# Performance work log

Measured on AMD Instinct MI355X. Metric: run time of the kernel, lower is better.

The kernel has to match this reference:

```python
import jax, jax.numpy as jnp
import numpy as np

B, K, V, NB = 256, 62, 14522, 28

def setup_inputs() -> dict:
    key = jax.random.key(0)
    ks = jax.random.split(key, 10)
    thetas = jax.random.normal(ks[0], (B, K * 3), dtype=jnp.float32) * 0.2
    bone_lengths_core = jax.random.normal(ks[1], (B, NB), dtype=jnp.float32)
    center_bone_length = jax.random.uniform(ks[2], (B, 1), dtype=jnp.float32) + 0.5
    trans = jax.random.normal(ks[3], (B, 3), dtype=jnp.float32)
    scale = jax.random.uniform(ks[4], (B,), dtype=jnp.float32) + 0.5
    v_template = jax.random.normal(ks[5], (V, 3), dtype=jnp.float32) * 0.05
    t_pose_joints = jax.random.normal(ks[6], (K, 3), dtype=jnp.float32) * 0.1
    weights = jax.nn.softmax(jax.random.normal(ks[7], (V, K), dtype=jnp.float32) * 2.0, axis=1)
    # kinematic tree: parent[i] < i (binary-ish tree), parent[0] unused
    parents = jnp.maximum((jnp.arange(K) - 1) // 2, 0).astype(jnp.int64)
    bone_length_mapper = jax.random.randint(ks[8], (K,), -1, NB).astype(jnp.int64)
    return {"thetas": thetas, "bone_lengths_core": bone_lengths_core,
            "center_bone_length": center_bone_length, "trans": trans, "scale": scale,
            "v_template": v_template, "t_pose_joints": t_pose_joints, "weights": weights,
            "parents": parents, "bone_length_mapper": bone_length_mapper}

def euler2mat(r):
    # r: [N,3] ZYX euler angles -> [N,3,3]
    z, y, x = r[:, 0], r[:, 1], r[:, 2]
    cx, sx = jnp.cos(x), jnp.sin(x)
    cy, sy = jnp.cos(y), jnp.sin(y)
    cz, sz = jnp.cos(z), jnp.sin(z)
    one = jnp.ones_like(x)
    zero = jnp.zeros_like(x)
    Rx = jnp.stack([one, zero, zero, zero, cx, -sx, zero, sx, cx], -1).reshape(-1, 3, 3)
    Ry = jnp.stack([cy, zero, sy, zero, one, zero, -sy, zero, cy], -1).reshape(-1, 3, 3)
    Rz = jnp.stack([cz, -sz, zero, sz, cz, zero, zero, zero, one], -1).reshape(-1, 3, 3)
    return jnp.einsum('nij,njk,nkl->nil', Rz, Ry, Rx)

def _forward(thetas, bone_lengths_core, center_bone_length, trans, scale,
             v_template, t_pose_joints, weights, parents, bone_length_mapper):
    b = thetas.shape[0]
    k = t_pose_joints.shape[0]
    blc = jax.nn.sigmoid(bone_lengths_core / 5.0) * 2.0          # [B,28]
    R = euler2mat(thetas.reshape(-1, 3)).reshape(b, k, 3, 3)      # [B,K,3,3]
    Jt = t_pose_joints                                            # [K,3]
    # per-joint bone-length scale factor [B,K]
    gathered = blc[:, jnp.clip(bone_length_mapper, 0)]            # [B,K]
    factor = jnp.where(bone_length_mapper[None, :] < 0, 1.0, gathered)
    factor = factor.at[:, 1].set(center_bone_length[:, 0])
    factor = factor.at[:, 0].set(1.0)
    # local translations: root uses J0, others scaled offsets to parent
    off = (Jt - Jt[parents])[None] * factor[:, :, None]           # [B,K,3]
    off = off.at[:, 0].set(Jt[0][None])
    # local affines A [B,K,4,4]
    A = jnp.zeros((b, k, 4, 4), dtype=thetas.dtype)
    A = A.at[:, :, :3, :3].set(R)
    A = A.at[:, :, :3, 3].set(off)
    A = A.at[:, :, 3, 3].set(1.0)
    # compose along the kinematic tree
    G0 = jnp.zeros_like(A).at[:, 0].set(A[:, 0])
    def step(G_all, i):
        Gp = jnp.take(G_all, parents[i], axis=1)                  # [B,4,4]
        Gi = Gp @ jnp.take(A, i, axis=1)
        return jax.lax.dynamic_update_index_in_dim(G_all, Gi, i, axis=1), None
    G_all, _ = jax.lax.scan(step, G0, jnp.arange(1, k))
    J_final = G_all[:, :, :3, 3]                                  # [B,K,3]
    # subtract inverse-bind contribution: G' = G - pack(G @ [J;0])
    RJ = jnp.einsum('bkij,kj->bki', G_all[:, :, :3, :3], Jt)
    G = G_all.at[:, :, :3, 3].add(-RJ)
    # LBS skinning: T [B,V,4,4]
    T = jnp.einsum('bkij,vk->bvij', G, weights)
    rest_h = jnp.concatenate([v_template, jnp.ones((v_template.shape[0], 1), v_template.dtype)], axis=1)
    v = jnp.einsum('bvij,vj->bvi', T, rest_h)[:, :, :3]
    V_final = v * scale[:, None, None] + trans[:, None, :]
    J_out = J_final * scale[:, None, None] + trans[:, None, :]
    return V_final, J_out

def reference(thetas, bone_lengths_core, center_bone_length, trans, scale,
              v_template, t_pose_joints, weights, parents, bone_length_mapper):
    return _forward(thetas, bone_lengths_core, center_bone_length, trans, scale,
                    v_template, t_pose_joints, weights, parents, bone_length_mapper)
```

## Files before the change

### kernel.cpp

```cpp
#include <hip/hip_runtime.h>

#define NBATCH 256
#define NJ     62
#define NV     14522
#define NCORE  28
#define KPAD   256
#define NN     768
#define MPAD   14528
#define OUTF   (NV * 3)
#define MT     908
#define NSTRIPE 128

typedef __attribute__((ext_vector_type(8))) short short8v;
typedef __attribute__((ext_vector_type(4))) short short4v;
typedef __attribute__((ext_vector_type(4))) float floatx4;
typedef __attribute__((ext_vector_type(2))) float floatx2;

#define AS1(p) ((const __attribute__((address_space(1))) void*)(p))
#define AS3(p) ((__attribute__((address_space(3))) void*)(p))

#define SCHED0() __builtin_amdgcn_sched_barrier(0)
#define WAITVM(n) do { SCHED0(); asm volatile("s_waitcnt vmcnt(" #n ")" ::: "memory"); SCHED0(); } while (0)

static __device__ inline short f2bf(float x) {
    unsigned u = __float_as_uint(x);
    unsigned r = (u + 0x7fffu + ((u >> 16) & 1u)) >> 16;
    return (short)r;
}

static __device__ inline unsigned swz(unsigned off) {
    return off ^ (((off >> 9) & 7u) << 4);
}

__global__ __launch_bounds__(256) void prep_kernel(
    const float* __restrict__ thetas, const float* __restrict__ blc,
    const float* __restrict__ cbl, const float* __restrict__ trans,
    const float* __restrict__ scale, const float* __restrict__ tpose,
    const int* __restrict__ parents, const int* __restrict__ mapper,
    const float* __restrict__ W, const float* __restrict__ vt,
    short* __restrict__ Bt, short* __restrict__ WH,
    float* __restrict__ Jout)
{
    __shared__ float Asm[4][NJ][12];
    __shared__ float Gsm[4][NJ][12];

    if (blockIdx.x >= 64) {
        const int id = (blockIdx.x - 64) * 256 + threadIdx.x;
        const int v = id >> 5;
        const int c = id & 31;
        const int k = c * 2;
        float w0 = 0.f, w1 = 0.f, hx = 0.f, hy = 0.f, hz = 0.f;
        if (v < NV) {
            hx = vt[v * 3 + 0]; hy = vt[v * 3 + 1]; hz = vt[v * 3 + 2];
            if (k < NJ)     w0 = W[(size_t)v * NJ + k];
            if (k + 1 < NJ) w1 = W[(size_t)v * NJ + k + 1];
        }
        short8v o;
        o[0] = f2bf(w0 * hx); o[1] = f2bf(w0 * hy); o[2] = f2bf(w0 * hz); o[3] = f2bf(w0);
        o[4] = f2bf(w1 * hx); o[5] = f2bf(w1 * hy); o[6] = f2bf(w1 * hz); o[7] = f2bf(w1);
        if (v < MPAD) *(short8v*)&WH[(size_t)v * KPAD + c * 8] = o;
        return;
    }

    const int w = threadIdx.x >> 6;
    const int b = blockIdx.x * 4 + w;
    const int k = threadIdx.x & 63;
    int p = 0;

    if (k < NJ) {
        p = parents[k];
        const float tz = thetas[(b * NJ + k) * 3 + 0];
        const float ty = thetas[(b * NJ + k) * 3 + 1];
        const float tx = thetas[(b * NJ + k) * 3 + 2];
        const float cx = cosf(tx), sx = sinf(tx);
        const float cy = cosf(ty), sy = sinf(ty);
        const float cz = cosf(tz), sz = sinf(tz);
        const float r00 = cz * cy;
        const float r01 = cz * sy * sx - sz * cx;
        const float r02 = sz * sx + cz * sy * cx;
        const float r10 = sz * cy;
        const float r11 = cz * cx + sz * sy * sx;
        const float r12 = sz * sy * cx - cz * sx;
        const float r20 = -sy;
        const float r21 = cy * sx;
        const float r22 = cy * cx;

        float f;
        const int m = mapper[k];
        if (k == 0)        f = 1.0f;
        else if (k == 1)   f = cbl[b];
        else if (m < 0)    f = 1.0f;
        else               f = 2.0f / (1.0f + expf(-blc[b * NCORE + m] * 0.2f));

        float ox, oy, oz;
        if (k == 0) {
            ox = tpose[0]; oy = tpose[1]; oz = tpose[2];
        } else {
            ox = (tpose[k * 3 + 0] - tpose[p * 3 + 0]) * f;
            oy = (tpose[k * 3 + 1] - tpose[p * 3 + 1]) * f;
            oz = (tpose[k * 3 + 2] - tpose[p * 3 + 2]) * f;
        }
        Asm[w][k][0] = r00; Asm[w][k][1] = r01; Asm[w][k][2]  = r02; Asm[w][k][3]  = ox;
        Asm[w][k][4] = r10; Asm[w][k][5] = r11; Asm[w][k][6]  = r12; Asm[w][k][7]  = oy;
        Asm[w][k][8] = r20; Asm[w][k][9] = r21; Asm[w][k][10] = r22; Asm[w][k][11] = oz;
    }
    __syncthreads();

    if (k == 0) {
        #pragma unroll
        for (int j = 0; j < 12; ++j) Gsm[w][0][j] = Asm[w][0][j];
    }
    __syncthreads();

    const int depth = (k < NJ) ? (31 - __clz((unsigned)(k + 1))) : 99;
    for (int d = 1; d <= 5; ++d) {
        if (depth == d) {
            float gp[12], a[12], g[12];
            #pragma unroll
            for (int j = 0; j < 12; ++j) { gp[j] = Gsm[w][p][j]; a[j] = Asm[w][k][j]; }
            #pragma unroll
            for (int i = 0; i < 3; ++i) {
                #pragma unroll
                for (int j = 0; j < 4; ++j) {
                    float s = (j == 3) ? gp[i * 4 + 3] : 0.0f;
                    s = fmaf(gp[i * 4 + 0], a[0 * 4 + j], s);
                    s = fmaf(gp[i * 4 + 1], a[1 * 4 + j], s);
                    s = fmaf(gp[i * 4 + 2], a[2 * 4 + j], s);
                    g[i * 4 + j] = s;
                }
            }
            #pragma unroll
            for (int j = 0; j < 12; ++j) Gsm[w][k][j] = g[j];
        }
        __syncthreads();
    }

    if (k < NJ) {
        float g[12];
        #pragma unroll
        for (int j = 0; j < 12; ++j) g[j] = Gsm[w][k][j];
        const float jx = tpose[k * 3 + 0];
        const float jy = tpose[k * 3 + 1];
        const float jz = tpose[k * 3 + 2];
        const float s  = scale[b];
        Jout[(b * NJ + k) * 3 + 0] = fmaf(g[3],  s, trans[b * 3 + 0]);
        Jout[(b * NJ + k) * 3 + 1] = fmaf(g[7],  s, trans[b * 3 + 1]);
        Jout[(b * NJ + k) * 3 + 2] = fmaf(g[11], s, trans[b * 3 + 2]);
        float np[3];
        np[0] = g[3]  - (g[0] * jx + g[1] * jy + g[2]  * jz);
        np[1] = g[7]  - (g[4] * jx + g[5] * jy + g[6]  * jz);
        np[2] = g[11] - (g[8] * jx + g[9] * jy + g[10] * jz);
        #pragma unroll
        for (int i = 0; i < 3; ++i) {
            short4v o;
            o[0] = f2bf(g[i * 4 + 0]);
            o[1] = f2bf(g[i * 4 + 1]);
            o[2] = f2bf(g[i * 4 + 2]);
            o[3] = f2bf(np[i]);
            *(short4v*)&Bt[(size_t)(b * 3 + i) * KPAD + k * 4] = o;
        }
        if (k == 0) {
            short4v z = {0, 0, 0, 0};
            #pragma unroll
            for (int i = 0; i < 3; ++i) {
                *(short4v*)&Bt[(size_t)(b * 3 + i) * KPAD + 248] = z;
                *(short4v*)&Bt[(size_t)(b * 3 + i) * KPAD + 252] = z;
            }
        }
    }
}

__global__ __launch_bounds__(256, 2) void gemm_skin(
    const short* __restrict__ WH,
    const short* __restrict__ Bt,
    const float* __restrict__ scale,
    const float* __restrict__ trans,
    float* __restrict__ out)
{
    __shared__ __align__(16) char lds_raw[65536 + 13312];

    const int tid  = threadIdx.x;
    const int wave = tid >> 6;
    const int lane = tid & 63;
    const int lrow = lane & 15;
    const int lk   = lane >> 4;
    const int y     = blockIdx.x >> 5;
    const int inner = blockIdx.x & 31;
    const int s     = inner * 4 + wave;
    const int ntiles = (s < (MT - 7 * NSTRIPE)) ? 8 : 7;
    const int b0 = y * 16;

    char* Ab0 = lds_raw + wave * 16384;
    char* Ab1 = Ab0 + 8192;
    float* epi = (float*)(lds_raw + 65536) + wave * 800;

    {
        const char* Bsrc = (const char*)(Bt + (size_t)y * 48 * KPAD);
        #pragma unroll
        for (int cc = 0; cc < 6; ++cc) {
            const unsigned Lb = (unsigned)(wave * 6144 + cc * 1024);
            __builtin_amdgcn_global_load_lds(AS1(Bsrc + swz(Lb + lane * 16)),
                                             AS3(lds_raw + Lb), 16, 0, 0);
        }
    }
    WAITVM(0);
    __syncthreads();

    short8v breg[3][8];
    #pragma unroll
    for (int nt = 0; nt < 3; ++nt) {
        const unsigned row = nt * 16 + lrow;
        const unsigned rb = row * 512, rx = (row & 7u) << 4;
        #pragma unroll
        for (int k8 = 0; k8 < 8; ++k8) {
            const unsigned cb = (unsigned)(k8 * 4 + lk) * 16;
            breg[nt][k8] = *(const short8v*)(lds_raw + rb + (cb ^ rx));
        }
    }
    __syncthreads();

    float sv[3], tv[3]; int bl3[3], ii3[3];
    #pragma unroll
    for (int nt = 0; nt < 3; ++nt) {
        const int n_loc = nt * 16 + lrow;
        bl3[nt] = n_loc / 3; ii3[nt] = n_loc - bl3[nt] * 3;
        sv[nt] = scale[b0 + bl3[nt]];
        tv[nt] = trans[(b0 + bl3[nt]) * 3 + ii3[nt]];
    }
    size_t sbase[6]; int loff[6], jj[6];
    #pragma unroll
    for (int it = 0; it < 6; ++it) {
        const int idx = it * 64 + lane;
        const int r = idx / 24, j = idx - r * 24;
        sbase[it] = (size_t)(b0 + r) * OUTF + 2 * j;
        loff[it]  = r * 50 + 2 * j;
        jj[it]    = j;
    }

    const unsigned arb = lrow * 512, arx = (lrow & 7u) << 4;
    const char* Asrc = (const char*)WH + (size_t)s * 8192;

    #pragma unroll
    for (int cc = 0; cc < 8; ++cc) {
        const unsigned Lb = cc * 1024;
        __builtin_amdgcn_global_load_lds(AS1(Asrc + swz(Lb + lane * 16)),
                                         AS3(Ab0 + Lb), 16, 0, 0);
    }
    WAITVM(0);

    for (int t = 0; t < ntiles; ++t) {
        char* bufR = (t & 1) ? Ab1 : Ab0;

        if (t + 1 < ntiles) {
            char* bufW = (t & 1) ? Ab0 : Ab1;
            const char* src = Asrc + (size_t)(t + 1) * (NSTRIPE * 8192);
            #pragma unroll
            for (int cc = 0; cc < 8; ++cc) {
                const unsigned Lb = cc * 1024;
                __builtin_amdgcn_global_load_lds(AS1(src + swz(Lb + lane * 16)),
                                                 AS3(bufW + Lb), 16, 0, 0);
            }
        }

        short8v af[8];
        #pragma unroll
        for (int k8 = 0; k8 < 8; ++k8) {
            const unsigned cb = (unsigned)(k8 * 4 + lk) * 16;
            af[k8] = *(const short8v*)(bufR + arb + (cb ^ arx));
        }
        floatx4 acc[3];
        #pragma unroll
        for (int nt = 0; nt < 3; ++nt) acc[nt] = (floatx4){0.f, 0.f, 0.f, 0.f};
        #pragma unroll
        for (int k8 = 0; k8 < 8; ++k8) {
            #pragma unroll
            for (int nt = 0; nt < 3; ++nt)
                acc[nt] = __builtin_amdgcn_mfma_f32_16x16x32_bf16(
                    af[k8], breg[nt][k8], acc[nt], 0, 0, 0);
        }

        #pragma unroll
        for (int nt = 0; nt < 3; ++nt) {
            #pragma unroll
            for (int r = 0; r < 4; ++r)
                epi[bl3[nt] * 50 + (lk * 4 + r) * 3 + ii3[nt]] =
                    fmaf(acc[nt][r], sv[nt], tv[nt]);
        }

        const int mtile = s + NSTRIPE * t;
        const int m48 = mtile * 48;
        const bool edge = (m48 + 48 > OUTF);
        #pragma unroll
        for (int it = 0; it < 6; ++it) {
            const floatx2 val = *(const floatx2*)&epi[loff[it]];
            if (!edge || m48 + 2 * jj[it] + 1 < OUTF)
                *(floatx2*)&out[sbase[it] + m48] = val;
        }

        if (t + 1 < ntiles) WAITVM(6);
    }
}

extern "C" void kernel_launch(void* const* d_in, const int* in_sizes, int n_in,
                              void* d_out, int out_size, void* d_ws, size_t ws_size,
                              hipStream_t stream)
{
    const float* thetas  = (const float*)d_in[0];
    const float* blc     = (const float*)d_in[1];
    const float* cbl     = (const float*)d_in[2];
    const float* trans   = (const float*)d_in[3];
    const float* scale   = (const float*)d_in[4];
    const float* vtempl  = (const float*)d_in[5];
    const float* tpose   = (const float*)d_in[6];
    const float* weights = (const float*)d_in[7];
    const int*   parents = (const int*)d_in[8];
    const int*   mapper  = (const int*)d_in[9];

    float* out  = (float*)d_out;
    float* Jout = out + (size_t)NBATCH * NV * 3;

    short* WH = (short*)d_ws;
    short* Bt = WH + (size_t)MPAD * KPAD;

    prep_kernel<<<64 + (MPAD * 32) / 256, 256, 0, stream>>>(
        thetas, blc, cbl, trans, scale, tpose, parents, mapper,
        weights, vtempl, Bt, WH, Jout);
    gemm_skin<<<512, 256, 0, stream>>>(WH, Bt, scale, trans, out);
}
```

Baseline: 28.95 us.

## Share A tile across waves in block and load B fragments directly from global

Result: slower. 31.82 us (+9.9%).

```diff
diff --git a/kernel.cpp b/kernel.cpp
--- a/kernel.cpp
+++ b/kernel.cpp
@@ -177,47 +177,33 @@
     const float* __restrict__ trans,
     float* __restrict__ out)
 {
-    __shared__ __align__(16) char lds_raw[65536 + 13312];
+    __shared__ __align__(16) char lds_raw[16384 + 4 * 3200];
 
     const int tid  = threadIdx.x;
     const int wave = tid >> 6;
     const int lane = tid & 63;
     const int lrow = lane & 15;
     const int lk   = lane >> 4;
-    const int y     = blockIdx.x >> 5;
-    const int inner = blockIdx.x & 31;
-    const int s     = inner * 4 + wave;
+    const int s    = blockIdx.x & 127;
+    const int g    = blockIdx.x >> 7;
+    const int yg   = g * 4 + wave;
+    const int b0   = yg * 16;
     const int ntiles = (s < (MT - 7 * NSTRIPE)) ? 8 : 7;
-    const int b0 = y * 16;
-
-    char* Ab0 = lds_raw + wave * 16384;
-    char* Ab1 = Ab0 + 8192;
-    float* epi = (float*)(lds_raw + 65536) + wave * 800;
-
+
+    char* Ab0 = lds_raw;
+    char* Ab1 = lds_raw + 8192;
+    float* epi = (float*)(lds_raw + 16384) + wave * 800;
+
+    short8v breg[3][8];
     {
-        const char* Bsrc = (const char*)(Bt + (size_t)y * 48 * KPAD);
-        #pragma unroll
-        for (int cc = 0; cc < 6; ++cc) {
-            const unsigned Lb = (unsigned)(wave * 6144 + cc * 1024);
-            __builtin_amdgcn_global_load_lds(AS1(Bsrc + swz(Lb + lane * 16)),
-                                             AS3(lds_raw + Lb), 16, 0, 0);
-        }
-    }
-    WAITVM(0);
-    __syncthreads();
-
-    short8v breg[3][8];
-    #pragma unroll
-    for (int nt = 0; nt < 3; ++nt) {
-        const unsigned row = nt * 16 + lrow;
-        const unsigned rb = row * 512, rx = (row & 7u) << 4;
-        #pragma unroll
-        for (int k8 = 0; k8 < 8; ++k8) {
-            const unsigned cb = (unsigned)(k8 * 4 + lk) * 16;
-            breg[nt][k8] = *(const short8v*)(lds_raw + rb + (cb ^ rx));
-        }
-    }
-    __syncthreads();
+        const short* Bw = Bt + (size_t)yg * 48 * KPAD;
+        #pragma unroll
+        for (int nt = 0; nt < 3; ++nt)
+            #pragma unroll
+            for (int k8 = 0; k8 < 8; ++k8)
+                breg[nt][k8] = *(const short8v*)(Bw + (nt * 16 + lrow) * KPAD
+                                                 + (k8 * 4 + lk) * 8);
+    }
 
     float sv[3], tv[3]; int bl3[3], ii3[3];
     #pragma unroll
@@ -241,12 +227,13 @@
     const char* Asrc = (const char*)WH + (size_t)s * 8192;
 
     #pragma unroll
-    for (int cc = 0; cc < 8; ++cc) {
-        const unsigned Lb = cc * 1024;
+    for (int c = 0; c < 2; ++c) {
+        const unsigned Lb = (unsigned)(wave * 2 + c) * 1024;
         __builtin_amdgcn_global_load_lds(AS1(Asrc + swz(Lb + lane * 16)),
                                          AS3(Ab0 + Lb), 16, 0, 0);
     }
     WAITVM(0);
+    __syncthreads();
 
     for (int t = 0; t < ntiles; ++t) {
         char* bufR = (t & 1) ? Ab1 : Ab0;
@@ -255,8 +242,8 @@
             char* bufW = (t & 1) ? Ab0 : Ab1;
             const char* src = Asrc + (size_t)(t + 1) * (NSTRIPE * 8192);
             #pragma unroll
-            for (int cc = 0; cc < 8; ++cc) {
-                const unsigned Lb = cc * 1024;
+            for (int c = 0; c < 2; ++c) {
+                const unsigned Lb = (unsigned)(wave * 2 + c) * 1024;
                 __builtin_amdgcn_global_load_lds(AS1(src + swz(Lb + lane * 16)),
                                                  AS3(bufW + Lb), 16, 0, 0);
             }
@@ -287,8 +274,7 @@
                     fmaf(acc[nt][r], sv[nt], tv[nt]);
         }
 
-        const int mtile = s + NSTRIPE * t;
-        const int m48 = mtile * 48;
+        const int m48 = (s + NSTRIPE * t) * 48;
         const bool edge = (m48 + 48 > OUTF);
         #pragma unroll
         for (int it = 0; it < 6; ++it) {
@@ -297,7 +283,10 @@
                 *(floatx2*)&out[sbase[it] + m48] = val;
         }
 
-        if (t + 1 < ntiles) WAITVM(6);
+        if (t + 1 < ntiles) {
+            WAITVM(6);
+            __syncthreads();
+        }
     }
 }
 
```
